# Performance work log

Hardware: AMD Instinct MI355X
Metric: run time of the kernel (lower is better)

The kernel has to match this reference:

```python
import jax, jax.numpy as jnp
import numpy as np

B, S, H, KVH, D, MD = 4, 4096, 2, 1, 2, 5  # batch, seq, heads, kv heads, head_dim, model_dim
EPS, SCALE = 1e-6, 16.0


def _rmsnorm(t):
    # RMSNormNoWeight with scale=16.0 over last dim
    var = jnp.mean(t * t, axis=-1, keepdims=True)
    return SCALE * t * jax.lax.rsqrt(var + EPS)


def _rope(t, cos, sin):
    # t: (B, S, h, D); cos/sin: (S, D//2). Complex multiply on interleaved pairs.
    tr, ti = t[..., 0::2], t[..., 1::2]
    c = cos[None, :, None, :]
    s = sin[None, :, None, :]
    out_r = tr * c - ti * s
    out_i = tr * s + ti * c
    return jnp.stack([out_r, out_i], axis=-1).reshape(t.shape)


def setup_inputs() -> dict:
    key = jax.random.key(0)
    ks = jax.random.split(key, 9)
    return {
        "x": jax.random.normal(ks[0], (B, S, MD), jnp.float32),
        "freqs": jax.random.normal(ks[1], (S, D // 2), jnp.float32),
        "shared_qk_v": jax.random.normal(ks[2], (MD,), jnp.float32),
        "shared_v_v": jax.random.normal(ks[3], (MD,), jnp.float32),
        "shared_o_v": jax.random.normal(ks[4], (H * D,), jnp.float32),
        "shared_vproj_u": jax.random.normal(ks[5], (KVH * D,), jnp.float32),
        "q_u": jax.random.normal(ks[6], (H * D,), jnp.float32),
        "k_u": jax.random.normal(ks[7], (KVH * D,), jnp.float32),
        "o_u": jax.random.normal(ks[8], (MD,), jnp.float32),
    }


def reference(x, freqs, shared_qk_v, shared_v_v, shared_o_v, shared_vproj_u, q_u, k_u, o_u):
    b, s = x.shape[0], x.shape[1]
    # rank-1 projections: (x . v) outer u
    s_qk = jnp.sum(x * shared_qk_v, axis=-1, keepdims=True)  # (B,S,1) shared by q and k
    q = (s_qk * q_u).reshape(b, s, H, D)
    k = (s_qk * k_u).reshape(b, s, KVH, D)
    s_v = jnp.sum(x * shared_v_v, axis=-1, keepdims=True)
    v = (s_v * shared_vproj_u).reshape(b, s, KVH, D)
    # qk-norm + rotary
    q = _rmsnorm(q)
    k = _rmsnorm(k)
    cos, sin = jnp.cos(freqs), jnp.sin(freqs)
    q = _rope(q, cos, sin)
    k = _rope(k, cos, sin)
    # (B,h,S,D)
    q = q.transpose(0, 2, 1, 3)
    k = k.transpose(0, 2, 1, 3)
    v = v.transpose(0, 2, 1, 3)
    # GQA repeat kv heads
    k = jnp.repeat(k, H // KVH, axis=1)
    v = jnp.repeat(v, H // KVH, axis=1)
    scores = jnp.einsum('bhqd,bhkd->bhqk', q, k) / jnp.sqrt(jnp.float32(D))
    probs = jax.nn.softmax(scores, axis=-1)
    out = jnp.einsum('bhqk,bhkd->bhqd', probs, v)
    out = out.transpose(0, 2, 1, 3).reshape(b, s, H * D)
    # rank-1 output projection
    s_o = jnp.sum(out * shared_o_v, axis=-1, keepdims=True)
    return s_o * o_u  # (B,S,MODEL_DIM)
```

## Files before the change

### kernel.cpp

```cpp
#include <hip/hip_runtime.h>
#include <math.h>


#define BQ 4
#define SQ 4096
#define MDQ 5
#define EPSQ 1e-6f
#define SCALEQ 16.0f
#define L2E 1.4426950408889634f
#define ISQ2 0.70710678118654752f

__device__ __forceinline__ float fast_exp2(float x) {
#if __has_builtin(__builtin_amdgcn_exp2f)
    return __builtin_amdgcn_exp2f(x);
#else
    return __expf(x * 0.6931471805599453f);
#endif
}

__global__ __launch_bounds__(256)
void ca_prep(const float* __restrict__ x, const float* __restrict__ freqs,
             const float* __restrict__ qk_v, const float* __restrict__ v_v,
             const float* __restrict__ k_u, float4* __restrict__ pqc)
{
    const int idx = blockIdx.x * 256 + threadIdx.x;
    const int j   = idx & (SQ - 1);

    const float w0 = k_u[0], w1 = k_u[1];
    const float mk = 0.5f * (w0 * w0 + w1 * w1);

    const float qk0 = qk_v[0], qk1 = qk_v[1], qk2 = qk_v[2], qk3 = qk_v[3], qk4 = qk_v[4];
    const float vv0 = v_v[0],  vv1 = v_v[1],  vv2 = v_v[2],  vv3 = v_v[3],  vv4 = v_v[4];

    const float* xr = x + (size_t)idx * MDQ;
    const float x0 = xr[0], x1 = xr[1], x2 = xr[2], x3 = xr[3], x4 = xr[4];
    const float a  = x0*qk0 + x1*qk1 + x2*qk2 + x3*qk3 + x4*qk4;
    const float sv = x0*vv0 + x1*vv1 + x2*vv2 + x3*vv3 + x4*vv4;

    float sj, cj;
    __sincosf(freqs[j], &sj, &cj);
    const float mu = SCALEQ * a * rsqrtf(a * a * mk + EPSQ);
    pqc[idx] = make_float4(mu * cj, mu * sj, sv, 0.0f);
}

#define BLOCK 256
#define RSETS 4
#define RPT 4
#define ROWSB (RSETS * RPT)
#define TILES (SQ / ROWSB)
#define KTILE 256
#define NKT (SQ / KTILE)
#define JPT (KTILE / 64)

__global__ __launch_bounds__(BLOCK)
void ca_main(const float* __restrict__ x,
             const float* __restrict__ freqs,
             const float* __restrict__ qk_v,
             const float* __restrict__ o_v,
             const float* __restrict__ vproj_u,
             const float* __restrict__ q_u,
             const float* __restrict__ k_u,
             const float* __restrict__ o_u,
             const float4* __restrict__ pqc,
             float* __restrict__ out)
{
    __shared__ float4 sKey[2][KTILE];

    const int tid = threadIdx.x;
    const int sp  = tid & 63;
    const int rs  = tid >> 6;
    const int bx  = blockIdx.x;
    const int b   = bx / TILES;
    const int tile = bx % TILES;
    const int i0  = tile * ROWSB + rs * RPT;

    const float w0 = k_u[0], w1 = k_u[1];
    const float mk  = 0.5f * (w0 * w0 + w1 * w1);
    const float Mmu = SCALEQ * rsqrtf(mk);

    const float qk0 = qk_v[0], qk1 = qk_v[1], qk2 = qk_v[2], qk3 = qk_v[3], qk4 = qk_v[4];
    const float u00 = q_u[0], u01 = q_u[1], u10 = q_u[2], u11 = q_u[3];
    const float m0 = 0.5f * (u00 * u00 + u01 * u01);
    const float m1 = 0.5f * (u10 * u10 + u11 * u11);
    const float A0 = u00 * w0 + u01 * w1, B0 = u01 * w0 - u00 * w1;
    const float A1 = u10 * w0 + u11 * w1, B1 = u11 * w0 - u10 * w1;

    float al0[RPT], be0[RPT], C0[RPT], al1[RPT], be1[RPT], C1[RPT];
#pragma unroll
    for (int k = 0; k < RPT; ++k) {
        const int i = i0 + k;
        const float* xi = x + (size_t)(b * SQ + i) * MDQ;
        const float ai = xi[0]*qk0 + xi[1]*qk1 + xi[2]*qk2 + xi[3]*qk3 + xi[4]*qk4;
        float si, ci;
        __sincosf(freqs[i], &si, &ci);
        const float lam0 = SCALEQ * ai * rsqrtf(ai * ai * m0 + EPSQ);
        const float lam1 = SCALEQ * ai * rsqrtf(ai * ai * m1 + EPSQ);
        const float a0  = lam0 * (A0 * ci - B0 * si) * ISQ2;
        const float b0_ = lam0 * (A0 * si + B0 * ci) * ISQ2;
        const float a1  = lam1 * (A1 * ci - B1 * si) * ISQ2;
        const float b1_ = lam1 * (A1 * si + B1 * ci) * ISQ2;
        const float r0 = sqrtf(a0 * a0 + b0_ * b0_);
        const float r1 = sqrtf(a1 * a1 + b1_ * b1_);
        al0[k] = a0 * L2E;  be0[k] = b0_ * L2E;  C0[k] = -r0 * Mmu * L2E;
        al1[k] = a1 * L2E;  be1[k] = b1_ * L2E;  C1[k] = -r1 * Mmu * L2E;
    }

    const float4* __restrict__ gsrc = pqc + (size_t)b * SQ + tid;

    float4 stage = gsrc[0];
    sKey[0][tid] = stage;
    __syncthreads();

    float l0[RPT], n0[RPT], l1[RPT], n1[RPT];
#pragma unroll
    for (int k = 0; k < RPT; ++k) { l0[k] = 0.f; n0[k] = 0.f; l1[k] = 0.f; n1[k] = 0.f; }

#pragma unroll 2
    for (int t = 0; t < NKT; ++t) {
        const int cur = t & 1;
        if (t + 1 < NKT) stage = gsrc[(size_t)(t + 1) * KTILE];

        const float4* kb = &sKey[cur][sp];
#pragma unroll
        for (int jj = 0; jj < JPT; ++jj) {
            const float4 v = kb[jj * 64];
#pragma unroll
            for (int k = 0; k < RPT; ++k) {
                const float s0 = fmaf(al0[k], v.x, fmaf(be0[k], v.y, C0[k]));
                const float s1 = fmaf(al1[k], v.x, fmaf(be1[k], v.y, C1[k]));
                const float e0 = fast_exp2(s0);
                const float e1 = fast_exp2(s1);
                l0[k] += e0;  n0[k] = fmaf(e0, v.z, n0[k]);
                l1[k] += e1;  n1[k] = fmaf(e1, v.z, n1[k]);
            }
        }

        if (t + 1 < NKT) {
            sKey[cur ^ 1][tid] = stage;
            __syncthreads();
        }
    }

#pragma unroll
    for (int m = 1; m < 64; m <<= 1) {
#pragma unroll
        for (int k = 0; k < RPT; ++k) {
            l0[k] += __shfl_xor(l0[k], m, 64);
            n0[k] += __shfl_xor(n0[k], m, 64);
            l1[k] += __shfl_xor(l1[k], m, 64);
            n1[k] += __shfl_xor(n1[k], m, 64);
        }
    }

    if (sp < RPT) {
        const int k = sp;
        const float L0 = fmaxf(l0[k], 1e-30f);
        const float L1 = fmaxf(l1[k], 1e-30f);
        const float W0 = n0[k] / L0, W1 = n1[k] / L1;

        const float p0 = vproj_u[0], p1 = vproj_u[1];
        const float d0 = p0 * o_v[0] + p1 * o_v[1];
        const float d1 = p0 * o_v[2] + p1 * o_v[3];
        const float so = W0 * d0 + W1 * d1;

        float* orow = out + (size_t)(b * SQ + i0 + k) * MDQ;
        orow[0] = so * o_u[0];
        orow[1] = so * o_u[1];
        orow[2] = so * o_u[2];
        orow[3] = so * o_u[3];
        orow[4] = so * o_u[4];
    }
}

#define FROWS 32
#define FSPLIT 8
#define FJSUB (SQ / FSPLIT)
#define FTILES (SQ / FROWS)

__global__ __launch_bounds__(256)
void ca_fallback(const float* __restrict__ x,
                 const float* __restrict__ freqs,
                 const float* __restrict__ qk_v,
                 const float* __restrict__ v_v,
                 const float* __restrict__ o_v,
                 const float* __restrict__ vproj_u,
                 const float* __restrict__ q_u,
                 const float* __restrict__ k_u,
                 const float* __restrict__ o_u,
                 float* __restrict__ out)
{
    __shared__ float2 sPQ[SQ];
    __shared__ float  sCv[SQ];
    __shared__ float4 sRed[FROWS][FSPLIT];

    const int tid  = threadIdx.x;
    const int b    = blockIdx.x / FTILES;
    const int tile = blockIdx.x % FTILES;

    const float w0 = k_u[0], w1 = k_u[1];
    const float mk  = 0.5f * (w0 * w0 + w1 * w1);
    const float Mmu = SCALEQ * rsqrtf(mk);

    const float qk0 = qk_v[0], qk1 = qk_v[1], qk2 = qk_v[2], qk3 = qk_v[3], qk4 = qk_v[4];
    const float vv0 = v_v[0],  vv1 = v_v[1],  vv2 = v_v[2],  vv3 = v_v[3],  vv4 = v_v[4];

    for (int k = 0; k < SQ / 256; ++k) {
        const int j = tid + k * 256;
        const float* xr = x + (size_t)(b * SQ + j) * MDQ;
        const float x0 = xr[0], x1 = xr[1], x2 = xr[2], x3 = xr[3], x4 = xr[4];
        const float a  = x0*qk0 + x1*qk1 + x2*qk2 + x3*qk3 + x4*qk4;
        const float sv = x0*vv0 + x1*vv1 + x2*vv2 + x3*vv3 + x4*vv4;
        float sj, cj;
        __sincosf(freqs[j], &sj, &cj);
        const float mu = SCALEQ * a * rsqrtf(a * a * mk + EPSQ);
        sPQ[j] = make_float2(mu * cj, mu * sj);
        sCv[j] = sv;
    }

    const int row = tid & (FROWS - 1);
    const int sp  = tid / FROWS;
    const int i   = tile * FROWS + row;

    const float u00 = q_u[0], u01 = q_u[1], u10 = q_u[2], u11 = q_u[3];
    const float m0 = 0.5f * (u00 * u00 + u01 * u01);
    const float m1 = 0.5f * (u10 * u10 + u11 * u11);
    const float A0 = u00 * w0 + u01 * w1, B0 = u01 * w0 - u00 * w1;
    const float A1 = u10 * w0 + u11 * w1, B1 = u11 * w0 - u10 * w1;

    const float* xi = x + (size_t)(b * SQ + i) * MDQ;
    const float ai = xi[0]*qk0 + xi[1]*qk1 + xi[2]*qk2 + xi[3]*qk3 + xi[4]*qk4;
    float si, ci;
    __sincosf(freqs[i], &si, &ci);
    const float lam0 = SCALEQ * ai * rsqrtf(ai * ai * m0 + EPSQ);
    const float lam1 = SCALEQ * ai * rsqrtf(ai * ai * m1 + EPSQ);
    const float alr0 = lam0 * (A0 * ci - B0 * si) * ISQ2;
    const float ber0 = lam0 * (A0 * si + B0 * ci) * ISQ2;
    const float alr1 = lam1 * (A1 * ci - B1 * si) * ISQ2;
    const float ber1 = lam1 * (A1 * si + B1 * ci) * ISQ2;
    const float r0 = sqrtf(alr0 * alr0 + ber0 * ber0);
    const float r1 = sqrtf(alr1 * alr1 + ber1 * ber1);
    const float al0 = alr0 * L2E, be0 = ber0 * L2E, C0 = -r0 * Mmu * L2E;
    const float al1 = alr1 * L2E, be1 = ber1 * L2E, C1 = -r1 * Mmu * L2E;

    __syncthreads();

    const float2* __restrict__ pq  = sPQ + sp * FJSUB;
    const float*  __restrict__ cvp = sCv + sp * FJSUB;
    float l0 = 0.f, n0 = 0.f, l1 = 0.f, n1 = 0.f;
#pragma unroll 8
    for (int jj = 0; jj < FJSUB; ++jj) {
        const float2 v = pq[jj];
        const float cv = cvp[jj];
        const float s0 = fmaf(al0, v.x, fmaf(be0, v.y, C0));
        const float s1 = fmaf(al1, v.x, fmaf(be1, v.y, C1));
        const float e0 = fast_exp2(s0);
        const float e1 = fast_exp2(s1);
        l0 += e0; n0 = fmaf(e0, cv, n0);
        l1 += e1; n1 = fmaf(e1, cv, n1);
    }

    sRed[row][sp] = make_float4(l0, n0, l1, n1);
    __syncthreads();

    if (tid < FROWS) {
        float L0 = 0.f, N0 = 0.f, L1 = 0.f, N1 = 0.f;
#pragma unroll
        for (int s = 0; s < FSPLIT; ++s) {
            const float4 t = sRed[tid][s];
            L0 += t.x; N0 += t.y; L1 += t.z; N1 += t.w;
        }
        L0 = fmaxf(L0, 1e-30f);
        L1 = fmaxf(L1, 1e-30f);
        const float W0 = N0 / L0, W1 = N1 / L1;
        const float p0 = vproj_u[0], p1 = vproj_u[1];
        const float d0 = p0 * o_v[0] + p1 * o_v[1];
        const float d1 = p0 * o_v[2] + p1 * o_v[3];
        const float so = W0 * d0 + W1 * d1;

        const int ig = tile * FROWS + tid;
        float* orow = out + (size_t)(b * SQ + ig) * MDQ;
        orow[0] = so * o_u[0];
        orow[1] = so * o_u[1];
        orow[2] = so * o_u[2];
        orow[3] = so * o_u[3];
        orow[4] = so * o_u[4];
    }
}

extern "C" void kernel_launch(void* const* d_in, const int* in_sizes, int n_in,
                              void* d_out, int out_size, void* d_ws, size_t ws_size,
                              hipStream_t stream) {
    (void)in_sizes; (void)n_in; (void)out_size;
    const float* x       = (const float*)d_in[0];
    const float* freqs   = (const float*)d_in[1];
    const float* qk_v    = (const float*)d_in[2];
    const float* v_v     = (const float*)d_in[3];
    const float* o_v     = (const float*)d_in[4];
    const float* vproj_u = (const float*)d_in[5];
    const float* q_u     = (const float*)d_in[6];
    const float* k_u     = (const float*)d_in[7];
    const float* o_u     = (const float*)d_in[8];
    float* out = (float*)d_out;

    const size_t pqc_bytes = (size_t)BQ * SQ * sizeof(float4);
    if (ws_size >= pqc_bytes) {
        float4* pqc = (float4*)d_ws;
        hipLaunchKernelGGL(ca_prep, dim3(BQ * SQ / 256), dim3(256), 0, stream,
                           x, freqs, qk_v, v_v, k_u, pqc);
        hipLaunchKernelGGL(ca_main, dim3(BQ * TILES), dim3(BLOCK), 0, stream,
                           x, freqs, qk_v, o_v, vproj_u, q_u, k_u, o_u, pqc, out);
    } else {
        hipLaunchKernelGGL(ca_fallback, dim3(BQ * FTILES), dim3(256), 0, stream,
                           x, freqs, qk_v, v_v, o_v, vproj_u, q_u, k_u, o_u, out);
    }
}
```

Baseline: 98.00 us.

## Pack two-head score math into v2f packed FMA and halve rows per thread

Rewrites the inner attention loop so the two heads' score, sum and weighted-sum math uses 2-wide float vectors, so the compiler can emit packed FP32 FMA/add/mul instructions. The key record now duplicates sv in its w slot to allow a packed multiply. Rows per thread drop from 4 to 2, which doubles the number of blocks and cuts registers per thread. It also removes the unroll-2 pragma on the tile loop. The risk is more global key reloads per row, and exp2 stays scalar.

```diff
diff --git a/kernel.cpp b/kernel.cpp
--- a/kernel.cpp
+++ b/kernel.cpp
@@ -10,6 +10,8 @@
 #define L2E 1.4426950408889634f
 #define ISQ2 0.70710678118654752f
 
+typedef float v2f __attribute__((ext_vector_type(2)));
+
 __device__ __forceinline__ float fast_exp2(float x) {
 #if __has_builtin(__builtin_amdgcn_exp2f)
     return __builtin_amdgcn_exp2f(x);
@@ -40,12 +42,12 @@
     float sj, cj;
     __sincosf(freqs[j], &sj, &cj);
     const float mu = SCALEQ * a * rsqrtf(a * a * mk + EPSQ);
-    pqc[idx] = make_float4(mu * cj, mu * sj, sv, 0.0f);
+    pqc[idx] = make_float4(mu * cj, mu * sj, sv, sv);
 }
 
 #define BLOCK 256
 #define RSETS 4
-#define RPT 4
+#define RPT 2
 #define ROWSB (RSETS * RPT)
 #define TILES (SQ / ROWSB)
 #define KTILE 256
@@ -85,7 +87,7 @@
     const float A0 = u00 * w0 + u01 * w1, B0 = u01 * w0 - u00 * w1;
     const float A1 = u10 * w0 + u11 * w1, B1 = u11 * w0 - u10 * w1;
 
-    float al0[RPT], be0[RPT], C0[RPT], al1[RPT], be1[RPT], C1[RPT];
+    v2f al[RPT], be[RPT], Cc[RPT];
 #pragma unroll
     for (int k = 0; k < RPT; ++k) {
         const int i = i0 + k;
@@ -101,8 +103,9 @@
         const float b1_ = lam1 * (A1 * si + B1 * ci) * ISQ2;
         const float r0 = sqrtf(a0 * a0 + b0_ * b0_);
         const float r1 = sqrtf(a1 * a1 + b1_ * b1_);
-        al0[k] = a0 * L2E;  be0[k] = b0_ * L2E;  C0[k] = -r0 * Mmu * L2E;
-        al1[k] = a1 * L2E;  be1[k] = b1_ * L2E;  C1[k] = -r1 * Mmu * L2E;
+        al[k] = (v2f){a0 * L2E, a1 * L2E};
+        be[k] = (v2f){b0_ * L2E, b1_ * L2E};
+        Cc[k] = (v2f){-r0 * Mmu * L2E, -r1 * Mmu * L2E};
     }
 
     const float4* __restrict__ gsrc = pqc + (size_t)b * SQ + tid;
@@ -111,11 +114,10 @@
     sKey[0][tid] = stage;
     __syncthreads();
 
-    float l0[RPT], n0[RPT], l1[RPT], n1[RPT];
-#pragma unroll
-    for (int k = 0; k < RPT; ++k) { l0[k] = 0.f; n0[k] = 0.f; l1[k] = 0.f; n1[k] = 0.f; }
-
-#pragma unroll 2
+    v2f l[RPT], n[RPT];
+#pragma unroll
+    for (int k = 0; k < RPT; ++k) { l[k] = (v2f){0.f, 0.f}; n[k] = (v2f){0.f, 0.f}; }
+
     for (int t = 0; t < NKT; ++t) {
         const int cur = t & 1;
         if (t + 1 < NKT) stage = gsrc[(size_t)(t + 1) * KTILE];
@@ -124,14 +126,17 @@
 #pragma unroll
         for (int jj = 0; jj < JPT; ++jj) {
             const float4 v = kb[jj * 64];
+            const v2f vx = (v2f){v.x, v.x};
+            const v2f vy = (v2f){v.y, v.y};
+            const v2f vz = (v2f){v.z, v.w};
 #pragma unroll
             for (int k = 0; k < RPT; ++k) {
-                const float s0 = fmaf(al0[k], v.x, fmaf(be0[k], v.y, C0[k]));
-                const float s1 = fmaf(al1[k], v.x, fmaf(be1[k], v.y, C1[k]));
-                const float e0 = fast_exp2(s0);
-                const float e1 = fast_exp2(s1);
-                l0[k] += e0;  n0[k] = fmaf(e0, v.z, n0[k]);
-                l1[k] += e1;  n1[k] = fmaf(e1, v.z, n1[k]);
+                const v2f s = al[k] * vx + (be[k] * vy + Cc[k]);
+                v2f e;
+                e.x = fast_exp2(s.x);
+                e.y = fast_exp2(s.y);
+                l[k] += e;
+                n[k] += e * vz;
             }
         }
 
@@ -145,18 +150,18 @@
     for (int m = 1; m < 64; m <<= 1) {
 #pragma unroll
         for (int k = 0; k < RPT; ++k) {
-            l0[k] += __shfl_xor(l0[k], m, 64);
-            n0[k] += __shfl_xor(n0[k], m, 64);
-            l1[k] += __shfl_xor(l1[k], m, 64);
-            n1[k] += __shfl_xor(n1[k], m, 64);
+            l[k].x += __shfl_xor(l[k].x, m, 64);
+            l[k].y += __shfl_xor(l[k].y, m, 64);
+            n[k].x += __shfl_xor(n[k].x, m, 64);
+            n[k].y += __shfl_xor(n[k].y, m, 64);
         }
     }
 
     if (sp < RPT) {
         const int k = sp;
-        const float L0 = fmaxf(l0[k], 1e-30f);
-        const float L1 = fmaxf(l1[k], 1e-30f);
-        const float W0 = n0[k] / L0, W1 = n1[k] / L1;
+        const float L0 = fmaxf(l[k].x, 1e-30f);
+        const float L1 = fmaxf(l[k].y, 1e-30f);
+        const float W0 = n[k].x / L0, W1 = n[k].y / L1;
 
         const float p0 = vproj_u[0], p1 = vproj_u[1];
         const float d0 = p0 * o_v[0] + p1 * o_v[1];
```

Result: faster. 92.92 us (-5.2%).
